# Kernel optimization log

Measured on AMD Instinct MI355X. Metric: run time of the kernel, lower is better.

## Reference

```python
import jax, jax.numpy as jnp
import numpy as np

PHI = 0.1  # fraction of pruned weights randomized per inference


def setup_inputs() -> dict:
    key = jax.random.key(0)
    k1, k2, k3 = jax.random.split(key, 3)
    d_out, d_in, batch = 8192, 8192, 256
    W = jax.random.normal(k1, (d_out, d_in), jnp.float32) * 0.02
    prune = jax.random.uniform(k2, (d_out, d_in)) < 0.9
    W = jnp.where(prune, 0.0, W)
    mask = (W == 0.0)  # _register_masks: pruned positions
    x = jax.random.normal(k3, (batch, d_in), jnp.float32)
    return {"x": x, "W": W, "mask": mask}


def reference(x, W, mask):
    # --- _apply_random_flip (vectorized) ---
    n_pruned = int(np.asarray(jnp.sum(mask)))          # concrete mask -> static count
    n_flip = max(1, int(PHI * n_pruned))
    keep = ~mask
    n_keep = jnp.sum(keep).astype(W.dtype)
    wk = jnp.where(keep, W, 0.0)
    mean = jnp.sum(wk) / n_keep
    # torch .std() is unbiased (n-1 denominator)
    var = jnp.sum(jnp.where(keep, (W - mean) ** 2, 0.0)) / (n_keep - 1.0)
    std = jnp.sqrt(var)
    key = jax.random.key(42)
    ks, kv = jax.random.split(key)
    # uniform random permutation of pruned indices -> top_k of random scores
    scores = jnp.where(mask.ravel(), jax.random.uniform(ks, (W.size,)), -1.0)
    _, flip_idx = jax.lax.top_k(scores, n_flip)        # [n_flip] flat indices into W
    vals = jax.random.normal(kv, (n_flip,), W.dtype) * std * 0.1
    W_flipped = W.ravel().at[flip_idx].set(vals).reshape(W.shape)
    # --- base_model forward (Linear, no bias) ---
    out = x @ W_flipped.T                               # [batch, d_out]
    # --- _restore_masks: zero flipped weights again (no effect on out) ---
    _ = jnp.where(mask, 0.0, W_flipped)
    return out
```

## Files before the change

### kernel.cpp

```cpp
#include <hip/hip_runtime.h>

typedef unsigned int u32;
typedef unsigned long long u64;
typedef unsigned short u16;

#define NTOT   67108864u
#define T0P    7399424u
#define PBASE  14452u
#define NSUP   1932u
#define NWSEG  4096u
#define WCAP   2176u
#define RCAP   4352u
#define KSPLIT 8
#define RBLK   512u
#define SEGPB  8

struct Scalars {
  double sumW;
  double sumW2;
  u64 npruned;
  u64 nflip;
  float stdf;
  float pad;
};

#define OFF_COLSUM 0ull
#define OFF_ALLOC  8192ull
#define OFF_SBASE  16384ull
#define OFF_SC     24576ull
#define OFF_SEGCNT 24704ull
#define OFF_BHIST  41216ull
#define OFF_BDEST  4235520ull
#define OFF_XBF    8429824ull
#define OFF_SEGS   12624128ull
#define OFF_ROUTED 48275712ull
#define OFF_WBF    81846400ull
#define WS_NEED_WBF 216064128ull
#define ROUTED_CAP 8388608u
#define OFF_OUTP   OFF_SEGS

__host__ __device__ inline void tf2x32(u32 k0, u32 k1, u32 x0, u32 x1, u32& y0, u32& y1) {
  u32 ks2 = k0 ^ k1 ^ 0x1BD11BDAu;
  x0 += k0; x1 += k1;
#define TFR(r) { x0 += x1; x1 = (x1 << (r)) | (x1 >> (32 - (r))); x1 ^= x0; }
  TFR(13) TFR(15) TFR(26) TFR(6)  x0 += k1;  x1 += ks2 + 1u;
  TFR(17) TFR(29) TFR(16) TFR(24) x0 += ks2; x1 += k0 + 2u;
  TFR(13) TFR(15) TFR(26) TFR(6)  x0 += k0;  x1 += k1 + 3u;
  TFR(17) TFR(29) TFR(16) TFR(24) x0 += k1;  x1 += ks2 + 4u;
  TFR(13) TFR(15) TFR(26) TFR(6)  x0 += ks2; x1 += k0 + 5u;
#undef TFR
  y0 = x0; y1 = x1;
}

__device__ inline u32 jax_bits32(u32 k0, u32 k1, u32 i) {
  u32 y0, y1; tf2x32(k0, k1, 0u, i, y0, y1);
  return y0 ^ y1;
}

__device__ inline u16 f2bf(float f) {
  union { float f; u32 u; } c; c.f = f;
  u32 r = ((c.u >> 16) & 1u) + 0x7FFFu;
  return (u16)((c.u + r) >> 16);
}

__device__ inline float erfinv32(float x) {
  float w = -log1pf(-x * x);
  float p;
  if (w < 5.0f) {
    w -= 2.5f;
    p = 2.81022636e-08f;
    p = fmaf(p, w, 3.43273939e-07f);
    p = fmaf(p, w, -3.5233877e-06f);
    p = fmaf(p, w, -4.39150654e-06f);
    p = fmaf(p, w, 0.00021858087f);
    p = fmaf(p, w, -0.00125372503f);
    p = fmaf(p, w, -0.00417768164f);
    p = fmaf(p, w, 0.246640727f);
    p = fmaf(p, w, 1.50140941f);
  } else {
    w = sqrtf(w) - 3.0f;
    p = -0.000200214257f;
    p = fmaf(p, w, 0.000100950558f);
    p = fmaf(p, w, 0.00134934322f);
    p = fmaf(p, w, -0.00367342844f);
    p = fmaf(p, w, 0.00573950773f);
    p = fmaf(p, w, -0.0076224613f);
    p = fmaf(p, w, 0.00943887047f);
    p = fmaf(p, w, 1.00167406f);
    p = fmaf(p, w, 2.83297682f);
  }
  return p * x;
}

__global__ __launch_bounds__(256) void k_pass1w(const float* __restrict__ W,
                                                u16* __restrict__ wbf, Scalars* sc,
                                                u32* segcnt, u32* segs,
                                                u32 uk0, u32 uk1) {
  u32 t = threadIdx.x;
  u32 bid = blockIdx.x;
  if (bid < 1024u) {
    u32 gid = bid * 256 + t;
    u32 lane = t & 63;
    u32 wid = gid >> 6;
    u32* wseg = segs + (u64)wid * WCAP;
    u32 wbase = 0;
    double s = 0.0, s2 = 0.0; u32 cnt = 0;
    const u32 stride4 = 1024u * 256u * 4u;
    for (u32 b4 = gid * 4; b4 < NTOT; b4 += stride4) {
      float4 w4 = *(const float4*)(W + b4);
      u32 sb0 = jax_bits32(uk0, uk1, b4 + 0) >> 9;
      u32 sb1 = jax_bits32(uk0, uk1, b4 + 1) >> 9;
      u32 sb2 = jax_bits32(uk0, uk1, b4 + 2) >> 9;
      u32 sb3 = jax_bits32(uk0, uk1, b4 + 3) >> 9;
      float we[4] = {w4.x, w4.y, w4.z, w4.w};
      u32 sbv[4] = {sb0, sb1, sb2, sb3};
      u32 cand[4]; u32 nc = 0;
#pragma unroll
      for (int e = 0; e < 4; e++) {
        float w = we[e];
        s  += (double)w;
        s2 += (double)w * (double)w;
        bool pr = (w == 0.0f);
        cnt += pr ? 1u : 0u;
        if (pr && sbv[e] >= T0P) { cand[nc] = b4 + e; nc++; }
      }
      u32 inc = nc;
#pragma unroll
      for (int o = 1; o < 64; o <<= 1) { u32 v = (u32)__shfl_up((int)inc, o); if (lane >= (u32)o) inc += v; }
      u32 tot = (u32)__shfl((int)inc, 63);
      u32 pos = wbase + inc - nc;
      for (u32 k2 = 0; k2 < nc; k2++)
        if (pos + k2 < WCAP) wseg[pos + k2] = cand[k2];
      wbase += tot;
    }
    for (int o = 32; o > 0; o >>= 1) {
      s += __shfl_down(s, o); s2 += __shfl_down(s2, o); cnt += __shfl_down(cnt, o);
    }
    if (lane == 0) {
      atomicAdd(&sc->sumW, s);
      atomicAdd(&sc->sumW2, s2);
      atomicAdd(&sc->npruned, (u64)cnt);
      segcnt[wid] = (wbase > WCAP) ? WCAP : wbase;
    }
  } else {
    u32 i0 = (bid - 1024u) * 256 + t;
    const u32 stride = 1024u * 256u;
    for (u32 g = i0; g < NTOT / 8; g += stride) {
      const float4* p = (const float4*)(W + (u64)g * 8);
      float4 a = p[0], b = p[1];
      uint4 o;
      o.x = (u32)f2bf(a.x) | ((u32)f2bf(a.y) << 16);
      o.y = (u32)f2bf(a.z) | ((u32)f2bf(a.w) << 16);
      o.z = (u32)f2bf(b.x) | ((u32)f2bf(b.y) << 16);
      o.w = (u32)f2bf(b.z) | ((u32)f2bf(b.w) << 16);
      *(uint4*)(wbf + (u64)g * 8) = o;
    }
  }
}

__global__ __launch_bounds__(256) void k_route_a(const u32* __restrict__ segs,
                                                 const u32* __restrict__ segcnt,
                                                 u32* bhist, u32 uk0, u32 uk1) {
  __shared__ u32 lhist[2048];
  u32 t = threadIdx.x;
  for (u32 j = t; j < 2048; j += 256) lhist[j] = 0;
  __syncthreads();
#pragma unroll 1
  for (int sg = 0; sg < SEGPB; sg++) {
    u32 wid = blockIdx.x * SEGPB + sg;
    u32 n = segcnt[wid]; if (n > WCAP) n = WCAP;
    const u32* sp = segs + (u64)wid * WCAP;
    for (u32 i = t; i < n; i += 256) {
      u32 sup = (jax_bits32(uk0, uk1, sp[i]) >> 18) - PBASE;
      atomicAdd(&lhist[sup], 1u);
    }
  }
  __syncthreads();
  for (u32 j = t; j < 2048; j += 256) bhist[blockIdx.x * 2048 + j] = lhist[j];
}

__global__ __launch_bounds__(256) void k_colscan(const u32* __restrict__ bhist,
                                                 u32* bdest, u32* colsum) {
  __shared__ u32 wtmp[4];
  u32 s = blockIdx.x, t = threadIdx.x, lane = t & 63, wv = t >> 6;
  u32 v0 = bhist[(t * 2 + 0) * 2048 + s];
  u32 v1 = bhist[(t * 2 + 1) * 2048 + s];
  u32 pr = v0 + v1;
  u32 inc = pr;
#pragma unroll
  for (int o = 1; o < 64; o <<= 1) { u32 x = (u32)__shfl_up((int)inc, o); if (lane >= (u32)o) inc += x; }
  if (lane == 63) wtmp[wv] = inc;
  __syncthreads();
  u32 woff = 0;
  for (u32 w = 0; w < wv; w++) woff += wtmp[w];
  u32 base = woff + inc - pr;
  bdest[(t * 2 + 0) * 2048 + s] = base;
  bdest[(t * 2 + 1) * 2048 + s] = base + v0;
  if (t == 255) colsum[s] = woff + inc;
}

__global__ __launch_bounds__(256) void k_scan(const u32* __restrict__ colsum, Scalars* sc,
                                              u32* alloc, u32* sbase) {
  __shared__ u32 h[2048];
  __shared__ u32 wtmp[4];
  u32 t = threadIdx.x, lane = t & 63, wv = t >> 6;
  for (u32 j = t; j < 2048; j += 256) h[j] = colsum[j];
  __syncthreads();
  {
    u32 a[8]; u32 s8 = 0;
#pragma unroll
    for (int k = 0; k < 8; k++) { a[k] = h[t * 8 + k]; s8 += a[k]; }
    u32 inc = s8;
#pragma unroll
    for (int o = 1; o < 64; o <<= 1) { u32 v = (u32)__shfl_up((int)inc, o); if (lane >= (u32)o) inc += v; }
    if (lane == 63) wtmp[wv] = inc;
    __syncthreads();
    u32 woff = 0; for (u32 w = 0; w < wv; w++) woff += wtmp[w];
    u32 base = woff + inc - s8;
#pragma unroll
    for (int k = 0; k < 8; k++) { alloc[t * 8 + k] = base; base += a[k]; }
    __syncthreads();
  }
  {
    u32 a[8]; u32 s8 = 0;
#pragma unroll
    for (int k = 0; k < 8; k++) { a[k] = h[2047 - (t * 8 + k)]; s8 += a[k]; }
    u32 inc = s8;
#pragma unroll
    for (int o = 1; o < 64; o <<= 1) { u32 v = (u32)__shfl_up((int)inc, o); if (lane >= (u32)o) inc += v; }
    if (lane == 63) wtmp[wv] = inc;
    __syncthreads();
    u32 woff = 0; for (u32 w = 0; w < wv; w++) woff += wtmp[w];
    u32 base = woff + inc - s8;
#pragma unroll
    for (int k = 0; k < 8; k++) { sbase[2047 - (t * 8 + k)] = base; base += a[k]; }
  }
  if (t == 0) {
    double nk = (double)NTOT - (double)sc->npruned;
    double mean = sc->sumW / nk;
    double var = (sc->sumW2 - 2.0 * mean * sc->sumW + nk * mean * mean) / (nk - 1.0);
    sc->stdf = (float)sqrt(var);
    u64 nfi = (u64)(0.1 * (double)sc->npruned);
    if (nfi < 1) nfi = 1;
    sc->nflip = nfi;
  }
}

__global__ __launch_bounds__(256) void k_route_b(const u32* __restrict__ segs,
                                                 const u32* __restrict__ segcnt,
                                                 const u32* __restrict__ alloc,
                                                 const u32* __restrict__ bdest,
                                                 u32* routed, u32 uk0, u32 uk1) {
  __shared__ u32 lcur[2048];
  u32 t = threadIdx.x;
  for (u32 j = t; j < 2048; j += 256) lcur[j] = alloc[j] + bdest[blockIdx.x * 2048 + j];
  __syncthreads();
#pragma unroll 1
  for (int sg = 0; sg < SEGPB; sg++) {
    u32 wid = blockIdx.x * SEGPB + sg;
    u32 n = segcnt[wid]; if (n > WCAP) n = WCAP;
    const u32* sp = segs + (u64)wid * WCAP;
    for (u32 i = t; i < n; i += 256) {
      u32 idx = sp[i];
      u32 sup = (jax_bits32(uk0, uk1, idx) >> 18) - PBASE;
      u32 pos = atomicAdd(&lcur[sup], 1u);
      if (pos < ROUTED_CAP) routed[pos] = idx;
    }
  }
}

__device__ inline void suf512(const u32* cnt, u32* suf, u32* wtmp) {
  u32 t = threadIdx.x, lane = t & 63, wv = t >> 6;
  u32 a0 = cnt[511 - t * 2], a1 = cnt[510 - t * 2];
  u32 s = a0 + a1;
  u32 inc = s;
#pragma unroll
  for (int o = 1; o < 64; o <<= 1) { u32 v = (u32)__shfl_up((int)inc, o); if (lane >= (u32)o) inc += v; }
  if (lane == 63) wtmp[wv] = inc;
  __syncthreads();
  u32 woff = 0;
  for (u32 w = 0; w < wv; w++) woff += wtmp[w];
  u32 base = woff + inc - s;
  suf[511 - t * 2] = base;
  suf[510 - t * 2] = base + a0;
  __syncthreads();
}

template<int WBF>
__global__ __launch_bounds__(256) void k_rank(float* __restrict__ W,
                                              u16* __restrict__ wbf,
                                              const u32* __restrict__ colsum,
                                              const u32* __restrict__ alloc,
                                              const u32* __restrict__ sbase,
                                              const u32* __restrict__ routed,
                                              const Scalars* __restrict__ sc,
                                              u32 uk0, u32 uk1, u32 vk0, u32 vk1) {
  u32 p = blockIdx.x;
  u32 n = colsum[p]; if (n == 0) return;
  if (n > RCAP) n = RCAP;
  u64 nflip = sc->nflip;
  u32 rbase = sbase[p];
  if ((u64)rbase >= nflip) return;
  __shared__ u32 sIdx[RCAP];
  __shared__ u16 sFine[RCAP];
  __shared__ u32 pIdx[RCAP];
  __shared__ u32 hist[512], gbase[512], cur[512], wtmp[4];
  u32 t = threadIdx.x;
  for (u32 j = t; j < 512; j += 256) hist[j] = 0;
  __syncthreads();
  const u32* src = routed + alloc[p];
  for (u32 i = t; i < n; i += 256) {
    u32 idx = src[i];
    u32 f = (jax_bits32(uk0, uk1, idx) >> 9) & 511u;
    sIdx[i] = idx;
    sFine[i] = (u16)f;
    atomicAdd(&hist[f], 1u);
  }
  __syncthreads();
  suf512(hist, gbase, wtmp);
  for (u32 j = t; j < 512; j += 256) cur[j] = gbase[j];
  __syncthreads();
  for (u32 i = t; i < n; i += 256) {
    u32 pos = atomicAdd(&cur[sFine[i]], 1u);
    pIdx[pos] = sIdx[i];
  }
  __syncthreads();
  float stdf = sc->stdf;
  for (u32 i = t; i < n; i += 256) {
    u32 f = sFine[i];
    u32 g0 = gbase[f], g1 = g0 + hist[f];
    u32 v = sIdx[i];
    u32 ord = 0;
    for (u32 q = g0; q < g1; q++) ord += (pIdx[q] < v) ? 1u : 0u;
    u64 rank = (u64)rbase + g0 + ord;
    if (rank >= nflip) continue;
    u32 bits = jax_bits32(vk0, vk1, (u32)rank);
    union { u32 u; float fl; } cv; cv.u = 0x3F800000u | (bits >> 9);
    float fu = cv.fl - 1.0f;
    const float lo = -0.99999994f;
    float u2 = fmaxf(lo, fu * 2.0f + lo);
    float nrm = 1.41421354f * erfinv32(u2);
    float val = (nrm * stdf) * 0.1f;
    if (WBF) wbf[v] = f2bf(val);
    else     W[v] = val;
  }
}

__global__ __launch_bounds__(256) void k_xconv(const float* __restrict__ x, u16* __restrict__ xbf) {
  u32 i = blockIdx.x * blockDim.x + threadIdx.x;
  float4 v = ((const float4*)x)[i];
  ushort4 o; o.x = f2bf(v.x); o.y = f2bf(v.y); o.z = f2bf(v.z); o.w = f2bf(v.w);
  ((ushort4*)xbf)[i] = o;
}

typedef __bf16 bf16x8 __attribute__((ext_vector_type(8)));
typedef float f32x4 __attribute__((ext_vector_type(4)));

__global__ __launch_bounds__(256, 3) void k_gemm2(const u16* __restrict__ xbf,
                                                  const u16* __restrict__ wbf,
                                                  float* __restrict__ outp) {
  __shared__ u16 As[128 * 64];
  __shared__ u16 Bs[128 * 64];
  u32 tid = threadIdx.x;
  u32 lane = tid & 63, wv = tid >> 6;
  u32 l8 = lane & 7;
  u32 lr = lane >> 3;
  u32 nrow = blockIdx.x * 128;
  u32 mrow = blockIdx.y * 128;
  u32 kbase = blockIdx.z * (8192u / KSPLIT);
  u32 wm = wv >> 1, wn = wv & 1;
  u32 r = lane & 15, q = lane >> 4;
  f32x4 acc[4][4];
#pragma unroll
  for (int i = 0; i < 4; i++)
#pragma unroll
    for (int j = 0; j < 4; j++) acc[i][j] = (f32x4){0.f, 0.f, 0.f, 0.f};

  for (u32 kb = kbase; kb < kbase + (8192u / KSPLIT); kb += 64u) {
#pragma unroll
    for (int j = 0; j < 4; j++) {
      u32 g = wv * 4 + (u32)j;
      u32 row = g * 8 + lr;
      u32 sc = ((l8 ^ (row & 7u)) * 8u);
      const u16* ga = xbf + (u64)(mrow + row) * 8192 + kb + sc;
      __builtin_amdgcn_global_load_lds((const u32*)ga, (u32*)&As[g * 512u], 16, 0, 0);
      const u16* gb = wbf + (u64)(nrow + row) * 8192 + kb + sc;
      __builtin_amdgcn_global_load_lds((const u32*)gb, (u32*)&Bs[g * 512u], 16, 0, 0);
    }
    __syncthreads();
#pragma unroll
    for (int ks = 0; ks < 2; ks++) {
      bf16x8 a[4], b[4];
      u32 ch = (u32)(ks * 4) + q;
#pragma unroll
      for (int mt = 0; mt < 4; mt++) {
        u32 row = wm * 64 + (u32)mt * 16 + r;
        a[mt] = *(bf16x8*)&As[row * 64 + ((ch ^ (r & 7u)) * 8u)];
      }
#pragma unroll
      for (int nt = 0; nt < 4; nt++) {
        u32 row = wn * 64 + (u32)nt * 16 + r;
        b[nt] = *(bf16x8*)&Bs[row * 64 + ((ch ^ (r & 7u)) * 8u)];
      }
#pragma unroll
      for (int mt = 0; mt < 4; mt++)
#pragma unroll
        for (int nt = 0; nt < 4; nt++)
          acc[mt][nt] = __builtin_amdgcn_mfma_f32_16x16x32_bf16(a[mt], b[nt], acc[mt][nt], 0, 0, 0);
    }
    __syncthreads();
  }
  float* op = outp + (u64)blockIdx.z * 2097152u;
  u32 quad = lane >> 4, col = lane & 15;
#pragma unroll
  for (int mt = 0; mt < 4; mt++)
#pragma unroll
    for (int nt = 0; nt < 4; nt++) {
      u32 n = nrow + wn * 64 + (u32)nt * 16 + col;
#pragma unroll
      for (int rg = 0; rg < 4; rg++) {
        u32 m = mrow + wm * 64 + (u32)mt * 16 + quad * 4 + (u32)rg;
        op[(u64)m * 8192 + n] = acc[mt][nt][rg];
      }
    }
}

__global__ __launch_bounds__(256) void k_redout(const float* __restrict__ part,
                                                float* __restrict__ out) {
  u32 i = blockIdx.x * 256 + threadIdx.x;
  float4 s = ((const float4*)part)[i];
#pragma unroll
  for (int k = 1; k < KSPLIT; k++) {
    float4 v = ((const float4*)(part + (u64)k * 2097152u))[i];
    s.x += v.x; s.y += v.y; s.z += v.z; s.w += v.w;
  }
  ((float4*)out)[i] = s;
}

__global__ __launch_bounds__(256, 2) void k_gemm_fb(const u16* __restrict__ xbf,
                                                    const float* __restrict__ W,
                                                    float* __restrict__ out) {
  __shared__ u16 xs[256 * 72];
  __shared__ u16 wsm[64 * 72];
  u32 tid = threadIdx.x;
  u32 lane = tid & 63, wv = tid >> 6;
  u32 nt0 = blockIdx.x * 64;
  u32 kbase = blockIdx.y * 2048u;
  f32x4 acc[4][4];
#pragma unroll
  for (int i = 0; i < 4; i++)
#pragma unroll
    for (int j = 0; j < 4; j++) acc[i][j] = (f32x4){0.f, 0.f, 0.f, 0.f};
  for (u32 kb = kbase; kb < kbase + 2048u; kb += 64u) {
#pragma unroll
    for (int r8 = 0; r8 < 8; r8++) {
      u32 row = r8 * 32 + (tid >> 3);
      u32 kseg = (tid & 7) * 8;
      uint4 v = *(const uint4*)(xbf + (u64)row * 8192 + kb + kseg);
      *(uint4*)&xs[row * 72 + kseg] = v;
    }
#pragma unroll
    for (int rr = 0; rr < 4; rr++) {
      u32 f4 = rr * 256 + tid;
      u32 row = f4 >> 4;
      u32 kc = (f4 & 15) * 4;
      float4 v = *(const float4*)(W + (u64)(nt0 + row) * 8192 + kb + kc);
      ushort4 o; o.x = f2bf(v.x); o.y = f2bf(v.y); o.z = f2bf(v.z); o.w = f2bf(v.w);
      *(ushort4*)&wsm[row * 72 + kc] = o;
    }
    __syncthreads();
#pragma unroll
    for (int ks = 0; ks < 2; ks++) {
      bf16x8 a[4], b[4];
      u32 koff = ks * 32 + (lane >> 4) * 8;
      u32 rsel = lane & 15;
#pragma unroll
      for (int mt = 0; mt < 4; mt++) a[mt] = *(bf16x8*)&xs[(wv * 64 + mt * 16 + rsel) * 72 + koff];
#pragma unroll
      for (int nt = 0; nt < 4; nt++) b[nt] = *(bf16x8*)&wsm[(nt * 16 + rsel) * 72 + koff];
#pragma unroll
      for (int mt = 0; mt < 4; mt++)
#pragma unroll
        for (int nt = 0; nt < 4; nt++)
          acc[mt][nt] = __builtin_amdgcn_mfma_f32_16x16x32_bf16(a[mt], b[nt], acc[mt][nt], 0, 0, 0);
    }
    __syncthreads();
  }
  u32 quad = lane >> 4, col = lane & 15;
#pragma unroll
  for (int mt = 0; mt < 4; mt++)
#pragma unroll
    for (int nt = 0; nt < 4; nt++) {
      u32 n = nt0 + nt * 16 + col;
#pragma unroll
      for (int rg = 0; rg < 4; rg++) {
        u32 m = wv * 64 + mt * 16 + quad * 4 + rg;
        atomicAdd(&out[(u64)m * 8192 + n], acc[mt][nt][rg]);
      }
    }
}

extern "C" void kernel_launch(void* const* d_in, const int* in_sizes, int n_in,
                              void* d_out, int out_size, void* d_ws, size_t ws_size,
                              hipStream_t stream) {
  const float* x; float* W;
  if (in_sizes[0] == 2097152) { x = (const float*)d_in[0]; W = (float*)d_in[1]; }
  else                        { x = (const float*)d_in[1]; W = (float*)d_in[0]; }
  float* out = (float*)d_out;
  char* ws = (char*)d_ws;

  u32* colsum = (u32*)(ws + OFF_COLSUM);
  u32* alloc  = (u32*)(ws + OFF_ALLOC);
  u32* sbase  = (u32*)(ws + OFF_SBASE);
  Scalars* sc = (Scalars*)(ws + OFF_SC);
  u32* segcnt = (u32*)(ws + OFF_SEGCNT);
  u32* bhist  = (u32*)(ws + OFF_BHIST);
  u32* bdest  = (u32*)(ws + OFF_BDEST);
  u16* xbf    = (u16*)(ws + OFF_XBF);
  u32* segs   = (u32*)(ws + OFF_SEGS);
  u32* routed = (u32*)(ws + OFF_ROUTED);
  u16* wbf    = (u16*)(ws + OFF_WBF);
  float* outp = (float*)(ws + OFF_OUTP);

  bool usewbf = (ws_size >= (size_t)WS_NEED_WBF);

  u32 a0, a1, b0, b1;
  tf2x32(0u, 42u, 0u, 0u, a0, a1);
  tf2x32(0u, 42u, 0u, 1u, b0, b1);

  hipMemsetAsync(sc, 0, sizeof(Scalars), stream);

  k_xconv<<<2048, 256, 0, stream>>>(x, xbf);
  k_pass1w<<<usewbf ? 2048 : 1024, 256, 0, stream>>>(W, wbf, sc, segcnt, segs, a0, a1);
  k_route_a<<<RBLK, 256, 0, stream>>>(segs, segcnt, bhist, a0, a1);
  k_colscan<<<2048, 256, 0, stream>>>(bhist, bdest, colsum);
  k_scan<<<1, 256, 0, stream>>>(colsum, sc, alloc, sbase);
  k_route_b<<<RBLK, 256, 0, stream>>>(segs, segcnt, alloc, bdest, routed, a0, a1);
  if (usewbf) {
    k_rank<1><<<NSUP, 256, 0, stream>>>(W, wbf, colsum, alloc, sbase, routed, sc, a0, a1, b0, b1);
    dim3 g(64, 2, KSPLIT);
    k_gemm2<<<g, 256, 0, stream>>>(xbf, wbf, outp);
    k_redout<<<2048, 256, 0, stream>>>(outp, out);
  } else {
    k_rank<0><<<NSUP, 256, 0, stream>>>(W, wbf, colsum, alloc, sbase, routed, sc, a0, a1, b0, b1);
    hipMemsetAsync(out, 0, (size_t)out_size * 4, stream);
    dim3 g(128, 4);
    k_gemm_fb<<<g, 256, 0, stream>>>(xbf, W, out);
  }
}
```

Measured before the change: 1.009 ms.

## Bucket flip writes by address before scattering into bf16 weights; float partial sums

Instead of writing each randomized bf16 value straight into the weight copy from the rank kernel in random order, the rank kernel now records (index, value) pairs in rank order. A bucketing kernel groups the pairs by high address bits, and a flip kernel then writes each bucket's entries into a localized region of the bf16 weights. The aim is to make the scattered 2-byte writes cache-friendly, at the cost of two extra kernels and tens of MB of intermediate traffic. Separately, the first pass accumulates its per-thread sums in float with fma instead of double, which cuts FP64 work but loses some precision in the mean and std statistics.

```diff
diff --git a/kernel.cpp b/kernel.cpp
--- a/kernel.cpp
+++ b/kernel.cpp
@@ -14,6 +14,10 @@
 #define KSPLIT 8
 #define RBLK   512u
 #define SEGPB  8
+#define NBKT   1024u
+#define BCAP   8192u
+#define FLIPCAP 6553600u
+#define BKTBLK 512u
 
 struct Scalars {
   double sumW;
@@ -36,6 +40,10 @@
 #define OFF_ROUTED 48275712ull
 #define OFF_WBF    81846400ull
 #define WS_NEED_WBF 216064128ull
+#define OFF_FLIPF  216064128ull
+#define OFF_FLIPB  268492928ull
+#define OFF_BCUR   335601792ull
+#define WS_NEED_T2 335605888ull
 #define ROUTED_CAP 8388608u
 #define OFF_OUTP   OFF_SEGS
 
@@ -104,7 +112,7 @@
     u32 wid = gid >> 6;
     u32* wseg = segs + (u64)wid * WCAP;
     u32 wbase = 0;
-    double s = 0.0, s2 = 0.0; u32 cnt = 0;
+    float sf = 0.f, sf2 = 0.f; u32 cnt = 0;
     const u32 stride4 = 1024u * 256u * 4u;
     for (u32 b4 = gid * 4; b4 < NTOT; b4 += stride4) {
       float4 w4 = *(const float4*)(W + b4);
@@ -118,8 +126,8 @@
 #pragma unroll
       for (int e = 0; e < 4; e++) {
         float w = we[e];
-        s  += (double)w;
-        s2 += (double)w * (double)w;
+        sf += w;
+        sf2 = fmaf(w, w, sf2);
         bool pr = (w == 0.0f);
         cnt += pr ? 1u : 0u;
         if (pr && sbv[e] >= T0P) { cand[nc] = b4 + e; nc++; }
@@ -133,6 +141,7 @@
         if (pos + k2 < WCAP) wseg[pos + k2] = cand[k2];
       wbase += tot;
     }
+    double s = (double)sf, s2 = (double)sf2;
     for (int o = 32; o > 0; o >>= 1) {
       s += __shfl_down(s, o); s2 += __shfl_down(s2, o); cnt += __shfl_down(cnt, o);
     }
@@ -286,9 +295,10 @@
   __syncthreads();
 }
 
-template<int WBF>
+template<int MODE>
 __global__ __launch_bounds__(256) void k_rank(float* __restrict__ W,
                                               u16* __restrict__ wbf,
+                                              u64* __restrict__ flipflat,
                                               const u32* __restrict__ colsum,
                                               const u32* __restrict__ alloc,
                                               const u32* __restrict__ sbase,
@@ -341,8 +351,57 @@
     float u2 = fmaxf(lo, fu * 2.0f + lo);
     float nrm = 1.41421354f * erfinv32(u2);
     float val = (nrm * stdf) * 0.1f;
-    if (WBF) wbf[v] = f2bf(val);
-    else     W[v] = val;
+    if (MODE == 2) {
+      if (rank < (u64)FLIPCAP) flipflat[rank] = ((u64)v << 16) | (u64)f2bf(val);
+    } else if (MODE == 1) {
+      wbf[v] = f2bf(val);
+    } else {
+      W[v] = val;
+    }
+  }
+}
+
+__global__ __launch_bounds__(256) void k_bkt(const u64* __restrict__ flipflat,
+                                             const Scalars* __restrict__ sc,
+                                             u64* __restrict__ flipbkt,
+                                             u32* __restrict__ bktcur) {
+  __shared__ u32 lh[NBKT];
+  __shared__ u32 lb[NBKT];
+  u32 t = threadIdx.x;
+  u32 nf = (u32)sc->nflip; if (nf > FLIPCAP) nf = FLIPCAP;
+  for (u32 j = t; j < NBKT; j += 256) lh[j] = 0;
+  __syncthreads();
+  u32 per = (nf + BKTBLK - 1u) / BKTBLK;
+  u32 lo = blockIdx.x * per;
+  u32 hi = lo + per; if (hi > nf) hi = nf;
+  for (u32 i = lo + t; i < hi; i += 256) {
+    u32 b = (u32)(flipflat[i] >> 32);
+    atomicAdd(&lh[b], 1u);
+  }
+  __syncthreads();
+  for (u32 j = t; j < NBKT; j += 256) {
+    u32 c = lh[j];
+    lb[j] = c ? atomicAdd(&bktcur[j], c) : 0u;
+    lh[j] = 0;
+  }
+  __syncthreads();
+  for (u32 i = lo + t; i < hi; i += 256) {
+    u64 pk = flipflat[i];
+    u32 b = (u32)(pk >> 32);
+    u32 pos = lb[b] + atomicAdd(&lh[b], 1u);
+    if (pos < BCAP) flipbkt[(u64)b * BCAP + pos] = pk;
+  }
+}
+
+__global__ __launch_bounds__(256) void k_flip(const u64* __restrict__ flipbkt,
+                                              const u32* __restrict__ bktcur,
+                                              u16* __restrict__ wbf) {
+  u32 b = blockIdx.x;
+  u32 n = bktcur[b]; if (n > BCAP) n = BCAP;
+  const u64* src = flipbkt + (u64)b * BCAP;
+  for (u32 i = threadIdx.x; i < n; i += 256) {
+    u64 pk = src[i];
+    wbf[(u32)((pk >> 16) & 0x3FFFFFFull)] = (u16)pk;
   }
 }
 
@@ -521,28 +580,40 @@
   u32* routed = (u32*)(ws + OFF_ROUTED);
   u16* wbf    = (u16*)(ws + OFF_WBF);
   float* outp = (float*)(ws + OFF_OUTP);
-
-  bool usewbf = (ws_size >= (size_t)WS_NEED_WBF);
+  u64* flipflat = (u64*)(ws + OFF_FLIPF);
+  u64* flipbkt  = (u64*)(ws + OFF_FLIPB);
+  u32* bktcur   = (u32*)(ws + OFF_BCUR);
+
+  bool t2 = (ws_size >= (size_t)WS_NEED_T2);
+  bool t1 = (ws_size >= (size_t)WS_NEED_WBF);
 
   u32 a0, a1, b0, b1;
   tf2x32(0u, 42u, 0u, 0u, a0, a1);
   tf2x32(0u, 42u, 0u, 1u, b0, b1);
 
   hipMemsetAsync(sc, 0, sizeof(Scalars), stream);
+  if (t2) hipMemsetAsync(bktcur, 0, NBKT * sizeof(u32), stream);
 
   k_xconv<<<2048, 256, 0, stream>>>(x, xbf);
-  k_pass1w<<<usewbf ? 2048 : 1024, 256, 0, stream>>>(W, wbf, sc, segcnt, segs, a0, a1);
+  k_pass1w<<<t1 ? 2048 : 1024, 256, 0, stream>>>(W, wbf, sc, segcnt, segs, a0, a1);
   k_route_a<<<RBLK, 256, 0, stream>>>(segs, segcnt, bhist, a0, a1);
   k_colscan<<<2048, 256, 0, stream>>>(bhist, bdest, colsum);
   k_scan<<<1, 256, 0, stream>>>(colsum, sc, alloc, sbase);
   k_route_b<<<RBLK, 256, 0, stream>>>(segs, segcnt, alloc, bdest, routed, a0, a1);
-  if (usewbf) {
-    k_rank<1><<<NSUP, 256, 0, stream>>>(W, wbf, colsum, alloc, sbase, routed, sc, a0, a1, b0, b1);
+  if (t2) {
+    k_rank<2><<<NSUP, 256, 0, stream>>>(W, wbf, flipflat, colsum, alloc, sbase, routed, sc, a0, a1, b0, b1);
+    k_bkt<<<BKTBLK, 256, 0, stream>>>(flipflat, sc, flipbkt, bktcur);
+    k_flip<<<NBKT, 256, 0, stream>>>(flipbkt, bktcur, wbf);
+    dim3 g(64, 2, KSPLIT);
+    k_gemm2<<<g, 256, 0, stream>>>(xbf, wbf, outp);
+    k_redout<<<2048, 256, 0, stream>>>(outp, out);
+  } else if (t1) {
+    k_rank<1><<<NSUP, 256, 0, stream>>>(W, wbf, flipflat, colsum, alloc, sbase, routed, sc, a0, a1, b0, b1);
     dim3 g(64, 2, KSPLIT);
     k_gemm2<<<g, 256, 0, stream>>>(xbf, wbf, outp);
     k_redout<<<2048, 256, 0, stream>>>(outp, out);
   } else {
-    k_rank<0><<<NSUP, 256, 0, stream>>>(W, wbf, colsum, alloc, sbase, routed, sc, a0, a1, b0, b1);
+    k_rank<0><<<NSUP, 256, 0, stream>>>(W, wbf, flipflat, colsum, alloc, sbase, routed, sc, a0, a1, b0, b1);
     hipMemsetAsync(out, 0, (size_t)out_size * 4, stream);
     dim3 g(128, 4);
     k_gemm_fb<<<g, 256, 0, stream>>>(xbf, W, out);
```

Result: slower. 1.170 ms (+16.0%).

## Split W pass into two halves, fuse x conversion, remap GEMM blocks per XCD

Applied to the files above, without the earlier changes.

The fp32 W statistics/candidate pass and the bf16 conversion are split into two kernels, each covering half of W. This is meant to let the conversion read W while it is still resident in cache from the stats pass. The separate x-conversion kernel is folded into the first pass kernel, and per-thread sums now use float accumulation instead of double. The GEMM launch is flattened to a 1-D grid whose block index is remapped so that blocks sharing a K-slice land on the same XCD, to improve L2 reuse. Float accumulation of sums risks precision loss in the mean and std estimate.

```diff
diff --git a/kernel.cpp b/kernel.cpp
--- a/kernel.cpp
+++ b/kernel.cpp
@@ -92,69 +92,101 @@
   return p * x;
 }
 
-__global__ __launch_bounds__(256) void k_pass1w(const float* __restrict__ W,
-                                                u16* __restrict__ wbf, Scalars* sc,
-                                                u32* segcnt, u32* segs,
-                                                u32 uk0, u32 uk1) {
-  u32 t = threadIdx.x;
-  u32 bid = blockIdx.x;
+__device__ inline void pass1_half(const float* __restrict__ W, Scalars* sc,
+                                  u32* segcnt, u32* segs, u32 uk0, u32 uk1,
+                                  u32 bid, u32 t, u32 lo, u32 hi, bool first) {
+  u32 gid = bid * 256 + t;
+  u32 lane = t & 63;
+  u32 wid = gid >> 6;
+  u32* wseg = segs + (u64)wid * WCAP;
+  u32 wbase = first ? 0u : segcnt[wid];
+  float sf = 0.f, sf2 = 0.f; u32 cnt = 0;
+  const u32 stride4 = 1024u * 256u * 4u;
+  for (u32 b4 = lo + gid * 4; b4 < hi; b4 += stride4) {
+    float4 w4 = *(const float4*)(W + b4);
+    u32 sb0 = jax_bits32(uk0, uk1, b4 + 0) >> 9;
+    u32 sb1 = jax_bits32(uk0, uk1, b4 + 1) >> 9;
+    u32 sb2 = jax_bits32(uk0, uk1, b4 + 2) >> 9;
+    u32 sb3 = jax_bits32(uk0, uk1, b4 + 3) >> 9;
+    float we[4] = {w4.x, w4.y, w4.z, w4.w};
+    u32 sbv[4] = {sb0, sb1, sb2, sb3};
+    u32 cand[4]; u32 nc = 0;
+#pragma unroll
+    for (int e = 0; e < 4; e++) {
+      float w = we[e];
+      sf += w;
+      sf2 = fmaf(w, w, sf2);
+      bool pr = (w == 0.0f);
+      cnt += pr ? 1u : 0u;
+      if (pr && sbv[e] >= T0P) { cand[nc] = b4 + e; nc++; }
+    }
+    u32 inc = nc;
+#pragma unroll
+    for (int o = 1; o < 64; o <<= 1) { u32 v = (u32)__shfl_up((int)inc, o); if (lane >= (u32)o) inc += v; }
+    u32 tot = (u32)__shfl((int)inc, 63);
+    u32 pos = wbase + inc - nc;
+    for (u32 k2 = 0; k2 < nc; k2++)
+      if (pos + k2 < WCAP) wseg[pos + k2] = cand[k2];
+    wbase += tot;
+  }
+  double s = (double)sf, s2 = (double)sf2;
+  for (int o = 32; o > 0; o >>= 1) {
+    s += __shfl_down(s, o); s2 += __shfl_down(s2, o); cnt += __shfl_down(cnt, o);
+  }
+  if (lane == 0) {
+    atomicAdd(&sc->sumW, s);
+    atomicAdd(&sc->sumW2, s2);
+    atomicAdd(&sc->npruned, (u64)cnt);
+    segcnt[wid] = first ? wbase : ((wbase > WCAP) ? WCAP : wbase);
+  }
+}
+
+__device__ inline void wconv_range(const float* __restrict__ W, u16* __restrict__ wbf,
+                                   u32 i0, u32 glo, u32 ghi) {
+  const u32 stride = 512u * 256u;
+  for (u32 g = glo + i0; g < ghi; g += stride) {
+    const float4* p = (const float4*)(W + (u64)g * 8);
+    float4 a = p[0], b = p[1];
+    uint4 o;
+    o.x = (u32)f2bf(a.x) | ((u32)f2bf(a.y) << 16);
+    o.y = (u32)f2bf(a.z) | ((u32)f2bf(a.w) << 16);
+    o.z = (u32)f2bf(b.x) | ((u32)f2bf(b.y) << 16);
+    o.w = (u32)f2bf(b.z) | ((u32)f2bf(b.w) << 16);
+    *(uint4*)(wbf + (u64)g * 8) = o;
+  }
+}
+
+__global__ __launch_bounds__(256) void k_pass1wA(const float* __restrict__ W,
+                                                 u16* __restrict__ wbf,
+                                                 const float* __restrict__ x,
+                                                 u16* __restrict__ xbf,
+                                                 Scalars* sc, u32* segcnt, u32* segs,
+                                                 u32 uk0, u32 uk1, u32 dowbf) {
+  u32 t = threadIdx.x, bid = blockIdx.x;
   if (bid < 1024u) {
-    u32 gid = bid * 256 + t;
-    u32 lane = t & 63;
-    u32 wid = gid >> 6;
-    u32* wseg = segs + (u64)wid * WCAP;
-    u32 wbase = 0;
-    double s = 0.0, s2 = 0.0; u32 cnt = 0;
-    const u32 stride4 = 1024u * 256u * 4u;
-    for (u32 b4 = gid * 4; b4 < NTOT; b4 += stride4) {
-      float4 w4 = *(const float4*)(W + b4);
-      u32 sb0 = jax_bits32(uk0, uk1, b4 + 0) >> 9;
-      u32 sb1 = jax_bits32(uk0, uk1, b4 + 1) >> 9;
-      u32 sb2 = jax_bits32(uk0, uk1, b4 + 2) >> 9;
-      u32 sb3 = jax_bits32(uk0, uk1, b4 + 3) >> 9;
-      float we[4] = {w4.x, w4.y, w4.z, w4.w};
-      u32 sbv[4] = {sb0, sb1, sb2, sb3};
-      u32 cand[4]; u32 nc = 0;
-#pragma unroll
-      for (int e = 0; e < 4; e++) {
-        float w = we[e];
-        s  += (double)w;
-        s2 += (double)w * (double)w;
-        bool pr = (w == 0.0f);
-        cnt += pr ? 1u : 0u;
-        if (pr && sbv[e] >= T0P) { cand[nc] = b4 + e; nc++; }
-      }
-      u32 inc = nc;
-#pragma unroll
-      for (int o = 1; o < 64; o <<= 1) { u32 v = (u32)__shfl_up((int)inc, o); if (lane >= (u32)o) inc += v; }
-      u32 tot = (u32)__shfl((int)inc, 63);
-      u32 pos = wbase + inc - nc;
-      for (u32 k2 = 0; k2 < nc; k2++)
-        if (pos + k2 < WCAP) wseg[pos + k2] = cand[k2];
-      wbase += tot;
-    }
-    for (int o = 32; o > 0; o >>= 1) {
-      s += __shfl_down(s, o); s2 += __shfl_down(s2, o); cnt += __shfl_down(cnt, o);
-    }
-    if (lane == 0) {
-      atomicAdd(&sc->sumW, s);
-      atomicAdd(&sc->sumW2, s2);
-      atomicAdd(&sc->npruned, (u64)cnt);
-      segcnt[wid] = (wbase > WCAP) ? WCAP : wbase;
-    }
+    pass1_half(W, sc, segcnt, segs, uk0, uk1, bid, t, 0u, NTOT / 2u, true);
+  } else if (bid < 1536u) {
+    if (dowbf) wconv_range(W, wbf, (bid - 1024u) * 256 + t, 0u, NTOT / 16u);
   } else {
-    u32 i0 = (bid - 1024u) * 256 + t;
-    const u32 stride = 1024u * 256u;
-    for (u32 g = i0; g < NTOT / 8; g += stride) {
-      const float4* p = (const float4*)(W + (u64)g * 8);
-      float4 a = p[0], b = p[1];
-      uint4 o;
-      o.x = (u32)f2bf(a.x) | ((u32)f2bf(a.y) << 16);
-      o.y = (u32)f2bf(a.z) | ((u32)f2bf(a.w) << 16);
-      o.z = (u32)f2bf(b.x) | ((u32)f2bf(b.y) << 16);
-      o.w = (u32)f2bf(b.z) | ((u32)f2bf(b.w) << 16);
-      *(uint4*)(wbf + (u64)g * 8) = o;
-    }
+    u32 i0 = (bid - 1536u) * 256 + t;
+    const u32 stride = 512u * 256u;
+    for (u32 g = i0; g < 524288u; g += stride) {
+      float4 v = ((const float4*)x)[g];
+      ushort4 o; o.x = f2bf(v.x); o.y = f2bf(v.y); o.z = f2bf(v.z); o.w = f2bf(v.w);
+      ((ushort4*)xbf)[g] = o;
+    }
+  }
+}
+
+__global__ __launch_bounds__(256) void k_pass1wB(const float* __restrict__ W,
+                                                 u16* __restrict__ wbf,
+                                                 Scalars* sc, u32* segcnt, u32* segs,
+                                                 u32 uk0, u32 uk1) {
+  u32 t = threadIdx.x, bid = blockIdx.x;
+  if (bid < 1024u) {
+    pass1_half(W, sc, segcnt, segs, uk0, uk1, bid, t, NTOT / 2u, NTOT, false);
+  } else {
+    wconv_range(W, wbf, (bid - 1024u) * 256 + t, NTOT / 16u, NTOT / 8u);
   }
 }
 
@@ -286,7 +318,7 @@
   __syncthreads();
 }
 
-template<int WBF>
+template<int MODE>
 __global__ __launch_bounds__(256) void k_rank(float* __restrict__ W,
                                               u16* __restrict__ wbf,
                                               const u32* __restrict__ colsum,
@@ -341,16 +373,9 @@
     float u2 = fmaxf(lo, fu * 2.0f + lo);
     float nrm = 1.41421354f * erfinv32(u2);
     float val = (nrm * stdf) * 0.1f;
-    if (WBF) wbf[v] = f2bf(val);
-    else     W[v] = val;
-  }
-}
-
-__global__ __launch_bounds__(256) void k_xconv(const float* __restrict__ x, u16* __restrict__ xbf) {
-  u32 i = blockIdx.x * blockDim.x + threadIdx.x;
-  float4 v = ((const float4*)x)[i];
-  ushort4 o; o.x = f2bf(v.x); o.y = f2bf(v.y); o.z = f2bf(v.z); o.w = f2bf(v.w);
-  ((ushort4*)xbf)[i] = o;
+    if (MODE == 1) wbf[v] = f2bf(val);
+    else           W[v] = val;
+  }
 }
 
 typedef __bf16 bf16x8 __attribute__((ext_vector_type(8)));
@@ -361,22 +386,27 @@
                                                   float* __restrict__ outp) {
   __shared__ u16 As[128 * 64];
   __shared__ u16 Bs[128 * 64];
+  u32 i = blockIdx.x;
+  u32 xcd = i & 7u, slot = i >> 3;
+  u32 mi = slot & 1u, qq = slot >> 1;
+  u32 pid = xcd * 64u + qq;
+  u32 kidx = pid >> 6;
+  u32 nb = pid & 63u;
+  u32 mrow = mi * 128u, nrow = nb * 128u;
+  u32 kbase = kidx * 1024u;
   u32 tid = threadIdx.x;
   u32 lane = tid & 63, wv = tid >> 6;
   u32 l8 = lane & 7;
   u32 lr = lane >> 3;
-  u32 nrow = blockIdx.x * 128;
-  u32 mrow = blockIdx.y * 128;
-  u32 kbase = blockIdx.z * (8192u / KSPLIT);
   u32 wm = wv >> 1, wn = wv & 1;
   u32 r = lane & 15, q = lane >> 4;
   f32x4 acc[4][4];
 #pragma unroll
-  for (int i = 0; i < 4; i++)
-#pragma unroll
-    for (int j = 0; j < 4; j++) acc[i][j] = (f32x4){0.f, 0.f, 0.f, 0.f};
-
-  for (u32 kb = kbase; kb < kbase + (8192u / KSPLIT); kb += 64u) {
+  for (int a = 0; a < 4; a++)
+#pragma unroll
+    for (int b = 0; b < 4; b++) acc[a][b] = (f32x4){0.f, 0.f, 0.f, 0.f};
+
+  for (u32 kb = kbase; kb < kbase + 1024u; kb += 64u) {
 #pragma unroll
     for (int j = 0; j < 4; j++) {
       u32 g = wv * 4 + (u32)j;
@@ -410,7 +440,7 @@
     }
     __syncthreads();
   }
-  float* op = outp + (u64)blockIdx.z * 2097152u;
+  float* op = outp + (u64)kidx * 2097152u;
   u32 quad = lane >> 4, col = lane & 15;
 #pragma unroll
   for (int mt = 0; mt < 4; mt++)
@@ -522,7 +552,7 @@
   u16* wbf    = (u16*)(ws + OFF_WBF);
   float* outp = (float*)(ws + OFF_OUTP);
 
-  bool usewbf = (ws_size >= (size_t)WS_NEED_WBF);
+  bool t1 = (ws_size >= (size_t)WS_NEED_WBF);
 
   u32 a0, a1, b0, b1;
   tf2x32(0u, 42u, 0u, 0u, a0, a1);
@@ -530,16 +560,15 @@
 
   hipMemsetAsync(sc, 0, sizeof(Scalars), stream);
 
-  k_xconv<<<2048, 256, 0, stream>>>(x, xbf);
-  k_pass1w<<<usewbf ? 2048 : 1024, 256, 0, stream>>>(W, wbf, sc, segcnt, segs, a0, a1);
+  k_pass1wA<<<2048, 256, 0, stream>>>(W, wbf, x, xbf, sc, segcnt, segs, a0, a1, t1 ? 1u : 0u);
+  k_pass1wB<<<t1 ? 1536 : 1024, 256, 0, stream>>>(W, wbf, sc, segcnt, segs, a0, a1);
   k_route_a<<<RBLK, 256, 0, stream>>>(segs, segcnt, bhist, a0, a1);
   k_colscan<<<2048, 256, 0, stream>>>(bhist, bdest, colsum);
   k_scan<<<1, 256, 0, stream>>>(colsum, sc, alloc, sbase);
   k_route_b<<<RBLK, 256, 0, stream>>>(segs, segcnt, alloc, bdest, routed, a0, a1);
-  if (usewbf) {
+  if (t1) {
     k_rank<1><<<NSUP, 256, 0, stream>>>(W, wbf, colsum, alloc, sbase, routed, sc, a0, a1, b0, b1);
-    dim3 g(64, 2, KSPLIT);
-    k_gemm2<<<g, 256, 0, stream>>>(xbf, wbf, outp);
+    k_gemm2<<<1024, 256, 0, stream>>>(xbf, wbf, outp);
     k_redout<<<2048, 256, 0, stream>>>(outp, out);
   } else {
     k_rank<0><<<NSUP, 256, 0, stream>>>(W, wbf, colsum, alloc, sbase, routed, sc, a0, a1, b0, b1);
```

Measured after the change: 1.134 ms. +12.3%, slower.
